# Optimization experiments

Measured on AMD Instinct MI355X. Metric: run time of the kernel, lower is better.

## Reference

```python
import jax, jax.numpy as jnp
import numpy as np

B, C, H, W = 32, 1536, 14, 14   # input is (B*4, C, H, W); joint -> (B, C, 2H, 2W)
CI = C // 2                     # non-local inter_channels
EPS = 1e-5


def conv1x1(x, w, b):
    # x: (b, cin, h, w); w: (cout, cin); b: (cout,)
    return jnp.einsum('bchw,oc->bohw', x, w) + b[None, :, None, None]


def maxpool2(x):
    b, c, h, w = x.shape
    return x.reshape(b, c, h // 2, 2, w // 2, 2).max(axis=(3, 5))


def setup_inputs():
    key = jax.random.key(0)
    ks = jax.random.split(key, 12)
    s = 0.02
    return {
        'x': jax.random.normal(ks[0], (B * 4, C, H, W), jnp.float32),
        'w_theta': jax.random.normal(ks[1], (CI, C), jnp.float32) * s,
        'b_theta': jnp.zeros((CI,), jnp.float32),
        'w_phi': jax.random.normal(ks[2], (CI, C), jnp.float32) * s,
        'b_phi': jnp.zeros((CI,), jnp.float32),
        'w_g': jax.random.normal(ks[3], (CI, C), jnp.float32) * s,
        'b_g': jnp.zeros((CI,), jnp.float32),
        'w_W': jax.random.normal(ks[4], (C, CI), jnp.float32) * s,
        'b_W': jnp.zeros((C,), jnp.float32),
        'bn_gamma': jax.random.normal(ks[5], (C,), jnp.float32) * 0.1 + 1.0,
        'bn_beta': jax.random.normal(ks[6], (C,), jnp.float32) * 0.1,
        'bn_mean': jax.random.normal(ks[7], (C,), jnp.float32) * 0.1,
        'bn_var': jnp.ones((C,), jnp.float32),
    }


def joint(x):
    # (B*4, C, H, W) -> (B, C, 2H, 2W): 4 views tiled in a 2x2 grid
    x4 = x.reshape(B, 4, C, H, W)
    top = jnp.concatenate([x4[:, 0], x4[:, 1]], axis=-1)   # (B, C, H, 2W)
    bot = jnp.concatenate([x4[:, 2], x4[:, 3]], axis=-1)
    return jnp.concatenate([top, bot], axis=-2)             # (B, C, 2H, 2W)


def reference(x, w_theta, b_theta, w_phi, b_phi, w_g, b_g, w_W, b_W,
              bn_gamma, bn_beta, bn_mean, bn_var):
    xj = joint(x)                                           # (B, C, Hj, Wj)
    b, c, hj, wj = xj.shape
    n = hj * wj                                             # 784 query positions

    theta = conv1x1(xj, w_theta, b_theta).reshape(b, CI, n)             # (B, CI, N)
    phi = maxpool2(conv1x1(xj, w_phi, b_phi)).reshape(b, CI, -1)        # (B, CI, N/4)
    g = maxpool2(conv1x1(xj, w_g, b_g)).reshape(b, CI, -1)              # (B, CI, N/4)

    f = jnp.einsum('bcn,bcm->bnm', theta, phi)              # (B, N, N/4)
    attn = jax.nn.softmax(f, axis=-1)
    y = jnp.einsum('bnm,bcm->bcn', attn, g)                 # (B, CI, N)
    y = y.reshape(b, CI, hj, wj)

    w_y = conv1x1(y, w_W, b_W)
    # BatchNorm (inference form)
    inv = jax.lax.rsqrt(bn_var + EPS)
    w_y = (w_y - bn_mean[None, :, None, None]) * (bn_gamma * inv)[None, :, None, None] \
          + bn_beta[None, :, None, None]
    return w_y + xj
```

## Files before the change

kernel.cpp:

```cpp
#include <hip/hip_runtime.h>
#include <hip/hip_bf16.h>

typedef __attribute__((ext_vector_type(8))) _Float16 f16x8;
typedef __attribute__((ext_vector_type(4))) float f32x4;
typedef __attribute__((ext_vector_type(4))) unsigned short us4;
typedef __attribute__((ext_vector_type(8))) unsigned short us8;

#define B_   32
#define C_   1536
#define CI_  768
#define N_   784
#define S_   196
#define MP_  224
#define MK_  196

__device__ __forceinline__ unsigned short f2h(float f) {
    _Float16 h = (_Float16)f;
    return __builtin_bit_cast(unsigned short, h);
}
__device__ __forceinline__ f32x4 mfma_f16(f16x8 a, f16x8 b, f32x4 c) {
    return __builtin_amdgcn_mfma_f32_16x16x32_f16(a, b, c, 0, 0, 0);
}
__device__ __forceinline__ void gl_lds16(const unsigned short* g, unsigned short* l) {
    __builtin_amdgcn_global_load_lds(
        (const __attribute__((address_space(1))) unsigned int*)g,
        (__attribute__((address_space(3))) unsigned int*)l, 16, 0, 0);
}

__global__ __launch_bounds__(256) void k_cvt(const float* __restrict__ src,
                                             unsigned short* __restrict__ dst,
                                             int count4) {
    int idx = blockIdx.x * 256 + threadIdx.x;
    if (idx < count4) {
        f32x4 v = ((const f32x4*)src)[idx];
        us4 o;
        o[0] = f2h(v[0]); o[1] = f2h(v[1]); o[2] = f2h(v[2]); o[3] = f2h(v[3]);
        ((us4*)dst)[idx] = o;
    }
}

__global__ __launch_bounds__(256) void k_build_xjT(const float* __restrict__ x,
                                                   unsigned short* __restrict__ xjT) {
    __shared__ __align__(16) unsigned short lds[196 * 40];
    int c0 = blockIdx.x * 32;
    int b4 = blockIdx.y;
    int b = b4 >> 2, v = b4 & 3;
    int tid = threadIdx.x;
    const float* src = x + ((size_t)b4 * C_ + c0) * S_;
    for (int idx = tid; idx < 32 * 49; idx += 256) {
        int cl = idx / 49;
        int sq = idx - cl * 49;
        f32x4 val = *(const f32x4*)(src + (size_t)cl * S_ + sq * 4);
        int s = sq * 4;
        lds[(s + 0) * 40 + cl] = f2h(val[0]);
        lds[(s + 1) * 40 + cl] = f2h(val[1]);
        lds[(s + 2) * 40 + cl] = f2h(val[2]);
        lds[(s + 3) * 40 + cl] = f2h(val[3]);
    }
    __syncthreads();
    int rowbase = (v >> 1) * 14, colbase = (v & 1) * 14;
    for (int idx = tid; idx < 196 * 4; idx += 256) {
        int s = idx >> 2, ch = idx & 3;
        int hh = s / 14, ww = s - hh * 14;
        int n = (rowbase + hh) * 28 + colbase + ww;
        us8 val = *(const us8*)(&lds[s * 40 + ch * 8]);
        *(us8*)(xjT + ((size_t)b * N_ + n) * C_ + c0 + ch * 8) = val;
    }
}

__global__ __launch_bounds__(256) void k_bnprep(const float* __restrict__ bw,
                                                const float* __restrict__ gamma,
                                                const float* __restrict__ beta,
                                                const float* __restrict__ mean,
                                                const float* __restrict__ var,
                                                float* __restrict__ scale,
                                                float* __restrict__ shift) {
    int i = blockIdx.x * 256 + threadIdx.x;
    if (i < C_) {
        float sc = gamma[i] * rsqrtf(var[i] + 1e-5f);
        scale[i] = sc;
        shift[i] = (bw[i] - mean[i]) * sc + beta[i];
    }
}

__global__ __launch_bounds__(256) void k_conv3(
    const unsigned short* __restrict__ xjT,
    const unsigned short* __restrict__ wf,
    const float* __restrict__ b_theta, const float* __restrict__ b_phi,
    const float* __restrict__ b_g,
    unsigned short* __restrict__ theta_T, unsigned short* __restrict__ phi_p,
    unsigned short* __restrict__ g_p) {
    __shared__ __align__(16) unsigned char smem[28672];
    unsigned short* A_s = (unsigned short*)smem;
    unsigned short* B_s = A_s + 128 * 32;
    float* fLDS = (float*)smem;

    int tn = blockIdx.x;
    int tm = blockIdx.y;
    int b  = blockIdx.z;
    int o0 = tm * 128, n0 = tn * 112;
    int region = o0 / 768;
    int obase = o0 - region * 768;
    const float* bias = (region == 0) ? b_theta : (region == 1) ? b_phi : b_g;

    int tid = threadIdx.x;
    int wv = tid >> 6, lane = tid & 63, lr = lane & 15, quad = lane >> 4;
    int l4r = lane >> 2, l4c = lane & 3;

    f32x4 acc[2][7];
#pragma unroll
    for (int i = 0; i < 2; ++i)
#pragma unroll
        for (int j = 0; j < 7; ++j) acc[i][j] = (f32x4){0.f, 0.f, 0.f, 0.f};

    const unsigned short* Arow = wf + (size_t)o0 * C_;
    const unsigned short* Brow = xjT + ((size_t)b * N_ + n0) * C_;

    for (int kk = 0; kk < 48; ++kk) {
        int k0 = kk * 32;
        for (int c = wv; c < 15; c += 4) {
            if (c < 8) {
                int row = c * 16 + l4r;
                gl_lds16(Arow + (size_t)row * C_ + k0 + l4c * 8, A_s + c * 512);
            } else {
                int cb = c - 8;
                int row = cb * 16 + l4r;
                gl_lds16(Brow + (size_t)row * C_ + k0 + l4c * 8, B_s + cb * 512);
            }
        }
        __syncthreads();
        f16x8 a0 = *(const f16x8*)(&A_s[((2 * wv + 0) * 16 + lr) * 32 + quad * 8]);
        f16x8 a1 = *(const f16x8*)(&A_s[((2 * wv + 1) * 16 + lr) * 32 + quad * 8]);
#pragma unroll
        for (int j = 0; j < 7; ++j) {
            f16x8 bb = *(const f16x8*)(&B_s[(j * 16 + lr) * 32 + quad * 8]);
            acc[0][j] = mfma_f16(a0, bb, acc[0][j]);
            acc[1][j] = mfma_f16(a1, bb, acc[1][j]);
        }
        __syncthreads();
    }

    for (int h = 0; h < 2; ++h) {
        if ((wv >> 1) == h) {
            int wrel = wv & 1;
#pragma unroll
            for (int i = 0; i < 2; ++i)
#pragma unroll
                for (int j = 0; j < 7; ++j)
#pragma unroll
                    for (int r = 0; r < 4; ++r) {
                        int o_rel = (wrel * 2 + i) * 16 + quad * 4 + r;
                        int n_l = j * 16 + lr;
                        fLDS[o_rel * 112 + n_l] = acc[i][j][r];
                    }
        }
        __syncthreads();
        if (region == 0) {
            for (int idx = tid; idx < 112 * 8; idx += 256) {
                int n_l = idx >> 3, ch = idx & 7;
                us8 outv;
#pragma unroll
                for (int k = 0; k < 8; ++k) {
                    int o_rel = ch * 8 + k;
                    float val = fLDS[o_rel * 112 + n_l] + bias[obase + h * 64 + o_rel];
                    outv[k] = f2h(val);
                }
                *(us8*)(theta_T + ((size_t)b * N_ + n0 + n_l) * CI_ + o0 + h * 64 + ch * 8) = outv;
            }
        } else if (region == 1) {
            for (int idx = tid; idx < 28 * 8; idx += 256) {
                int mm = idx >> 3, ch = idx & 7;
                int a = mm / 14, mw = mm - a * 14;
                int m = (tn * 2 + a) * 14 + mw;
                int sb = a * 56 + mw * 2;
                us8 outv;
#pragma unroll
                for (int k = 0; k < 8; ++k) {
                    int o_rel = ch * 8 + k;
                    const float* p = &fLDS[o_rel * 112 + sb];
                    float val = fmaxf(fmaxf(p[0], p[1]), fmaxf(p[28], p[29]));
                    val += bias[obase + h * 64 + o_rel];
                    outv[k] = f2h(val);
                }
                *(us8*)(phi_p + ((size_t)b * MP_ + m) * CI_ + obase + h * 64 + ch * 8) = outv;
            }
        } else {
            for (int idx = tid; idx < 128; idx += 256) {
                int o_rel = idx >> 1, a = idx & 1;
                int ci = obase + h * 64 + o_rel;
                unsigned short* dst = g_p + ((size_t)b * CI_ + ci) * MP_ + (tn * 2 + a) * 14;
                const float* p0 = &fLDS[o_rel * 112 + a * 56];
                float bv = bias[obase + h * 64 + o_rel];
#pragma unroll
                for (int mw = 0; mw < 14; ++mw) {
                    const float* p = p0 + mw * 2;
                    dst[mw] = f2h(fmaxf(fmaxf(p[0], p[1]), fmaxf(p[28], p[29])) + bv);
                }
            }
        }
        __syncthreads();
    }
}

__global__ __launch_bounds__(256) void k_attn(
    const unsigned short* __restrict__ theta_T,
    const unsigned short* __restrict__ phi_p,
    const unsigned short* __restrict__ g_p,
    unsigned short* __restrict__ y) {
    __shared__ __align__(16) float f_s[32 * 228];

    int nb = blockIdx.x, b = blockIdx.y;
    int n0 = nb * 32;
    int tid = threadIdx.x, wv = tid >> 6, lane = tid & 63, lr = lane & 15, quad = lane >> 4;
    int mf0 = wv * 4;
    int nm = (mf0 + 4 <= 14) ? 4 : (14 - mf0);

    int na0 = n0 + lr;       if (na0 > 783) na0 = 783;
    int na1 = n0 + 16 + lr;  if (na1 > 783) na1 = 783;
    const unsigned short* tA0 = theta_T + ((size_t)b * N_ + na0) * CI_ + quad * 8;
    const unsigned short* tA1 = theta_T + ((size_t)b * N_ + na1) * CI_ + quad * 8;

    f32x4 acc[2][4];
#pragma unroll
    for (int i = 0; i < 2; ++i)
#pragma unroll
        for (int j = 0; j < 4; ++j) acc[i][j] = (f32x4){0.f, 0.f, 0.f, 0.f};

    for (int kk = 0; kk < 24; ++kk) {
        int k0 = kk * 32;
        f16x8 a0 = *(const f16x8*)(tA0 + k0);
        f16x8 a1 = *(const f16x8*)(tA1 + k0);
        for (int j = 0; j < nm; ++j) {
            f16x8 bb = *(const f16x8*)(phi_p +
                ((size_t)b * MP_ + (mf0 + j) * 16 + lr) * CI_ + k0 + quad * 8);
            acc[0][j] = mfma_f16(a0, bb, acc[0][j]);
            acc[1][j] = mfma_f16(a1, bb, acc[1][j]);
        }
    }
    for (int i = 0; i < 2; ++i)
        for (int j = 0; j < nm; ++j)
#pragma unroll
            for (int r = 0; r < 4; ++r)
                f_s[(i * 16 + quad * 4 + r) * 228 + (mf0 + j) * 16 + lr] = acc[i][j][r];
    __syncthreads();
    if (tid < 32) {
        float* row = f_s + tid * 228;
        float mx = -1e30f;
        for (int m = 0; m < MK_; ++m) mx = fmaxf(mx, row[m]);
        float sum = 0.f;
        for (int m = 0; m < MK_; ++m) { float e = __expf(row[m] - mx); row[m] = e; sum += e; }
        float inv = 1.0f / sum;
        for (int m = 0; m < MK_; ++m) row[m] *= inv;
        for (int m = MK_; m < MP_; ++m) row[m] = 0.f;
    }
    __syncthreads();
    for (int c3 = 0; c3 < 3; ++c3) {
        int ci0 = c3 * 256;
        f32x4 acc2[2][4];
#pragma unroll
        for (int i = 0; i < 2; ++i)
#pragma unroll
            for (int j = 0; j < 4; ++j) acc2[i][j] = (f32x4){0.f, 0.f, 0.f, 0.f};
        for (int km = 0; km < 7; ++km) {
            int k0 = km * 32;
            f16x8 a[2];
#pragma unroll
            for (int i = 0; i < 2; ++i) {
                const float* fp = &f_s[(i * 16 + lr) * 228 + k0 + quad * 8];
                f16x8 t;
#pragma unroll
                for (int j = 0; j < 8; ++j) t[j] = (_Float16)fp[j];
                a[i] = t;
            }
#pragma unroll
            for (int j = 0; j < 4; ++j) {
                f16x8 bb = *(const f16x8*)(g_p +
                    ((size_t)b * CI_ + ci0 + (wv * 4 + j) * 16 + lr) * MP_ + k0 + quad * 8);
                acc2[0][j] = mfma_f16(a[0], bb, acc2[0][j]);
                acc2[1][j] = mfma_f16(a[1], bb, acc2[1][j]);
            }
        }
#pragma unroll
        for (int i = 0; i < 2; ++i)
#pragma unroll
            for (int j = 0; j < 4; ++j)
#pragma unroll
                for (int r = 0; r < 4; ++r) {
                    int n = n0 + i * 16 + quad * 4 + r;
                    if (n < N_) {
                        int ci = ci0 + (wv * 4 + j) * 16 + lr;
                        y[((size_t)b * N_ + n) * CI_ + ci] = f2h(acc2[i][j][r]);
                    }
                }
    }
}

__global__ __launch_bounds__(256) void k_final(
    const unsigned short* __restrict__ yb,
    const unsigned short* __restrict__ wfW,
    const float* __restrict__ scale, const float* __restrict__ shift,
    const float* __restrict__ x,
    float* __restrict__ out) {
    __shared__ __align__(16) unsigned short smem_us[128 * 32 + 112 * 32];
    unsigned short* A_s = smem_us;
    unsigned short* B_s = smem_us + 128 * 32;
    int tn = blockIdx.x, tm = blockIdx.y, b = blockIdx.z;
    int o0 = tm * 128, n0 = tn * 112;
    int tid = threadIdx.x, wv = tid >> 6, lane = tid & 63, lr = lane & 15, quad = lane >> 4;
    int l4r = lane >> 2, l4c = lane & 3;

    f32x4 acc[2][7];
#pragma unroll
    for (int i = 0; i < 2; ++i)
#pragma unroll
        for (int j = 0; j < 7; ++j) acc[i][j] = (f32x4){0.f, 0.f, 0.f, 0.f};

    const unsigned short* Arow = wfW + (size_t)o0 * CI_;
    const unsigned short* Brow = yb + ((size_t)b * N_ + n0) * CI_;

    for (int kk = 0; kk < 24; ++kk) {
        int k0 = kk * 32;
        for (int c = wv; c < 15; c += 4) {
            if (c < 8) {
                int row = c * 16 + l4r;
                gl_lds16(Arow + (size_t)row * CI_ + k0 + l4c * 8, A_s + c * 512);
            } else {
                int cb = c - 8;
                int row = cb * 16 + l4r;
                gl_lds16(Brow + (size_t)row * CI_ + k0 + l4c * 8, B_s + cb * 512);
            }
        }
        __syncthreads();
        f16x8 a0 = *(const f16x8*)(&A_s[((2 * wv + 0) * 16 + lr) * 32 + quad * 8]);
        f16x8 a1 = *(const f16x8*)(&A_s[((2 * wv + 1) * 16 + lr) * 32 + quad * 8]);
#pragma unroll
        for (int j = 0; j < 7; ++j) {
            f16x8 bb = *(const f16x8*)(&B_s[(j * 16 + lr) * 32 + quad * 8]);
            acc[0][j] = mfma_f16(a0, bb, acc[0][j]);
            acc[1][j] = mfma_f16(a1, bb, acc[1][j]);
        }
        __syncthreads();
    }
#pragma unroll
    for (int i = 0; i < 2; ++i)
#pragma unroll
        for (int r = 0; r < 4; ++r) {
            int o = o0 + (2 * wv + i) * 16 + quad * 4 + r;
            float sc = scale[o], sh = shift[o];
#pragma unroll
            for (int j = 0; j < 7; ++j) {
                int n = n0 + j * 16 + lr;
                int hh = n / 28, ww = n - hh * 28;
                int vv = ((hh >= 14) ? 2 : 0) + ((ww >= 14) ? 1 : 0);
                int s = (hh - ((hh >= 14) ? 14 : 0)) * 14 + (ww - ((ww >= 14) ? 14 : 0));
                float xval = x[((size_t)(b * 4 + vv) * C_ + o) * S_ + s];
                out[((size_t)b * C_ + o) * N_ + n] = acc[i][j][r] * sc + sh + xval;
            }
        }
}

extern "C" void kernel_launch(void* const* d_in, const int* in_sizes, int n_in,
                              void* d_out, int out_size, void* d_ws, size_t ws_size,
                              hipStream_t stream) {
    (void)in_sizes; (void)n_in; (void)out_size; (void)ws_size;
    const float* x       = (const float*)d_in[0];
    const float* w_theta = (const float*)d_in[1];
    const float* b_theta = (const float*)d_in[2];
    const float* w_phi   = (const float*)d_in[3];
    const float* b_phi   = (const float*)d_in[4];
    const float* w_g     = (const float*)d_in[5];
    const float* b_g     = (const float*)d_in[6];
    const float* w_W     = (const float*)d_in[7];
    const float* b_W     = (const float*)d_in[8];
    const float* gamma   = (const float*)d_in[9];
    const float* beta    = (const float*)d_in[10];
    const float* mean    = (const float*)d_in[11];
    const float* var     = (const float*)d_in[12];

    char* ob = (char*)d_out;
    unsigned short* xjT     = (unsigned short*)(ob);
    unsigned short* theta_T = (unsigned short*)(ob + 77070336);
    unsigned short* phi_p   = (unsigned short*)(ob + 115605504);
    unsigned short* g_p     = (unsigned short*)(ob + 126615552);
    unsigned short* wf3     = (unsigned short*)(ob + 137625600);

    char* ws = (char*)d_ws;
    unsigned short* yb    = (unsigned short*)(ws);
    unsigned short* wfW   = (unsigned short*)(ws + 38535168);
    float*          scale = (float*)(ws + 40894464);
    float*          shift = (float*)(ws + 40900608);

    hipMemsetAsync(phi_p, 0, 11010048, stream);
    hipMemsetAsync(g_p, 0, 11010048, stream);

    k_bnprep<<<6, 256, 0, stream>>>(b_W, gamma, beta, mean, var, scale, shift);
    k_cvt<<<1152, 256, 0, stream>>>(w_theta, wf3,                294912);
    k_cvt<<<1152, 256, 0, stream>>>(w_phi,   wf3 + 768 * 1536,   294912);
    k_cvt<<<1152, 256, 0, stream>>>(w_g,     wf3 + 2 * 768 * 1536, 294912);
    k_cvt<<<1152, 256, 0, stream>>>(w_W,     wfW,                294912);
    k_build_xjT<<<dim3(48, 128), 256, 0, stream>>>(x, xjT);
    k_conv3<<<dim3(7, 18, 32), 256, 0, stream>>>(xjT, wf3, b_theta, b_phi, b_g,
                                                 theta_T, phi_p, g_p);
    k_attn<<<dim3(25, 32), 256, 0, stream>>>(theta_T, phi_p, g_p, yb);
    k_final<<<dim3(7, 12, 32), 256, 0, stream>>>(yb, wfW, scale, shift, x,
                                                 (float*)d_out);
}
```

Before: 882.7 us.

## Double-buffer LDS staging with XOR swizzle in GEMMs and parallelize softmax rows

Both 1x1-conv GEMM kernels now use two LDS buffers, so the global-to-LDS load of the next K slice is issued before computing on the current one. This replaces the load/sync/compute/sync serialization. An XOR swizzle on the 16-byte column chunk is applied to reads and writes to reduce LDS bank conflicts. The attention softmax now spreads each row over 8 threads with shuffle reductions instead of 32 serial threads, which costs more LDS and relies on the async loads completing before the barrier.

```diff
diff --git a/kernel.cpp b/kernel.cpp
--- a/kernel.cpp
+++ b/kernel.cpp
@@ -25,6 +25,23 @@
     __builtin_amdgcn_global_load_lds(
         (const __attribute__((address_space(1))) unsigned int*)g,
         (__attribute__((address_space(3))) unsigned int*)l, 16, 0, 0);
+}
+
+__device__ __forceinline__ void stage15(const unsigned short* Arow,
+                                        const unsigned short* Brow,
+                                        unsigned short* A_s, unsigned short* B_s,
+                                        int k0, int stride,
+                                        int wv, int l4r, int l4c_sw) {
+    for (int c = wv; c < 15; c += 4) {
+        if (c < 8) {
+            gl_lds16(Arow + (size_t)(c * 16 + l4r) * stride + k0 + l4c_sw * 8,
+                     A_s + c * 512);
+        } else {
+            int cb = c - 8;
+            gl_lds16(Brow + (size_t)(cb * 16 + l4r) * stride + k0 + l4c_sw * 8,
+                     B_s + cb * 512);
+        }
+    }
 }
 
 __global__ __launch_bounds__(256) void k_cvt(const float* __restrict__ src,
@@ -83,6 +100,18 @@
     }
 }
 
+#define COMPUTE_STEP(As, Bs)                                                     \
+    {                                                                            \
+        f16x8 a0 = *(const f16x8*)(&(As)[((2 * wv + 0) * 16 + lr) * 32 + rcol]); \
+        f16x8 a1 = *(const f16x8*)(&(As)[((2 * wv + 1) * 16 + lr) * 32 + rcol]); \
+        _Pragma("unroll")                                                        \
+        for (int j = 0; j < 7; ++j) {                                            \
+            f16x8 bb = *(const f16x8*)(&(Bs)[(j * 16 + lr) * 32 + rcol]);        \
+            acc[0][j] = mfma_f16(a0, bb, acc[0][j]);                             \
+            acc[1][j] = mfma_f16(a1, bb, acc[1][j]);                             \
+        }                                                                        \
+    }
+
 __global__ __launch_bounds__(256) void k_conv3(
     const unsigned short* __restrict__ xjT,
     const unsigned short* __restrict__ wf,
@@ -90,9 +119,11 @@
     const float* __restrict__ b_g,
     unsigned short* __restrict__ theta_T, unsigned short* __restrict__ phi_p,
     unsigned short* __restrict__ g_p) {
-    __shared__ __align__(16) unsigned char smem[28672];
-    unsigned short* A_s = (unsigned short*)smem;
-    unsigned short* B_s = A_s + 128 * 32;
+    __shared__ __align__(16) unsigned char smem[30720];
+    unsigned short* A0 = (unsigned short*)smem;
+    unsigned short* B0 = A0 + 4096;
+    unsigned short* A1 = A0 + 7680;
+    unsigned short* B1 = A0 + 11776;
     float* fLDS = (float*)smem;
 
     int tn = blockIdx.x;
@@ -106,6 +137,8 @@
     int tid = threadIdx.x;
     int wv = tid >> 6, lane = tid & 63, lr = lane & 15, quad = lane >> 4;
     int l4r = lane >> 2, l4c = lane & 3;
+    int l4c_sw = l4c ^ ((l4r >> 1) & 3);
+    int rcol = (quad ^ ((lr >> 1) & 3)) * 8;
 
     f32x4 acc[2][7];
 #pragma unroll
@@ -116,27 +149,15 @@
     const unsigned short* Arow = wf + (size_t)o0 * C_;
     const unsigned short* Brow = xjT + ((size_t)b * N_ + n0) * C_;
 
-    for (int kk = 0; kk < 48; ++kk) {
-        int k0 = kk * 32;
-        for (int c = wv; c < 15; c += 4) {
-            if (c < 8) {
-                int row = c * 16 + l4r;
-                gl_lds16(Arow + (size_t)row * C_ + k0 + l4c * 8, A_s + c * 512);
-            } else {
-                int cb = c - 8;
-                int row = cb * 16 + l4r;
-                gl_lds16(Brow + (size_t)row * C_ + k0 + l4c * 8, B_s + cb * 512);
-            }
-        }
-        __syncthreads();
-        f16x8 a0 = *(const f16x8*)(&A_s[((2 * wv + 0) * 16 + lr) * 32 + quad * 8]);
-        f16x8 a1 = *(const f16x8*)(&A_s[((2 * wv + 1) * 16 + lr) * 32 + quad * 8]);
-#pragma unroll
-        for (int j = 0; j < 7; ++j) {
-            f16x8 bb = *(const f16x8*)(&B_s[(j * 16 + lr) * 32 + quad * 8]);
-            acc[0][j] = mfma_f16(a0, bb, acc[0][j]);
-            acc[1][j] = mfma_f16(a1, bb, acc[1][j]);
-        }
+    stage15(Arow, Brow, A0, B0, 0, C_, wv, l4r, l4c_sw);
+    __syncthreads();
+    for (int kk = 0; kk < 48; kk += 2) {
+        stage15(Arow, Brow, A1, B1, (kk + 1) * 32, C_, wv, l4r, l4c_sw);
+        COMPUTE_STEP(A0, B0);
+        __syncthreads();
+        if (kk + 2 < 48)
+            stage15(Arow, Brow, A0, B0, (kk + 2) * 32, C_, wv, l4r, l4c_sw);
+        COMPUTE_STEP(A1, B1);
         __syncthreads();
     }
 
@@ -243,15 +264,30 @@
             for (int r = 0; r < 4; ++r)
                 f_s[(i * 16 + quad * 4 + r) * 228 + (mf0 + j) * 16 + lr] = acc[i][j][r];
     __syncthreads();
-    if (tid < 32) {
-        float* row = f_s + tid * 228;
+    {
+        int row = tid >> 3, sub = tid & 7;
+        float* rowp = f_s + row * 228;
+        int m0 = sub * 28;
         float mx = -1e30f;
-        for (int m = 0; m < MK_; ++m) mx = fmaxf(mx, row[m]);
+#pragma unroll
+        for (int m = 0; m < 28; ++m)
+            if (m0 + m < MK_) mx = fmaxf(mx, rowp[m0 + m]);
+        mx = fmaxf(mx, __shfl_xor(mx, 1));
+        mx = fmaxf(mx, __shfl_xor(mx, 2));
+        mx = fmaxf(mx, __shfl_xor(mx, 4));
         float sum = 0.f;
-        for (int m = 0; m < MK_; ++m) { float e = __expf(row[m] - mx); row[m] = e; sum += e; }
+#pragma unroll
+        for (int m = 0; m < 28; ++m) {
+            float e = (m0 + m < MK_) ? __expf(rowp[m0 + m] - mx) : 0.f;
+            rowp[m0 + m] = e;
+            sum += e;
+        }
+        sum += __shfl_xor(sum, 1);
+        sum += __shfl_xor(sum, 2);
+        sum += __shfl_xor(sum, 4);
         float inv = 1.0f / sum;
-        for (int m = 0; m < MK_; ++m) row[m] *= inv;
-        for (int m = MK_; m < MP_; ++m) row[m] = 0.f;
+#pragma unroll
+        for (int m = 0; m < 28; ++m) rowp[m0 + m] *= inv;
     }
     __syncthreads();
     for (int c3 = 0; c3 < 3; ++c3) {
@@ -301,13 +337,17 @@
     const float* __restrict__ scale, const float* __restrict__ shift,
     const float* __restrict__ x,
     float* __restrict__ out) {
-    __shared__ __align__(16) unsigned short smem_us[128 * 32 + 112 * 32];
-    unsigned short* A_s = smem_us;
-    unsigned short* B_s = smem_us + 128 * 32;
+    __shared__ __align__(16) unsigned short smem_us[2 * (128 * 32 + 112 * 32)];
+    unsigned short* A0 = smem_us;
+    unsigned short* B0 = smem_us + 4096;
+    unsigned short* A1 = smem_us + 7680;
+    unsigned short* B1 = smem_us + 11776;
     int tn = blockIdx.x, tm = blockIdx.y, b = blockIdx.z;
     int o0 = tm * 128, n0 = tn * 112;
     int tid = threadIdx.x, wv = tid >> 6, lane = tid & 63, lr = lane & 15, quad = lane >> 4;
     int l4r = lane >> 2, l4c = lane & 3;
+    int l4c_sw = l4c ^ ((l4r >> 1) & 3);
+    int rcol = (quad ^ ((lr >> 1) & 3)) * 8;
 
     f32x4 acc[2][7];
 #pragma unroll
@@ -318,27 +358,15 @@
     const unsigned short* Arow = wfW + (size_t)o0 * CI_;
     const unsigned short* Brow = yb + ((size_t)b * N_ + n0) * CI_;
 
-    for (int kk = 0; kk < 24; ++kk) {
-        int k0 = kk * 32;
-        for (int c = wv; c < 15; c += 4) {
-            if (c < 8) {
-                int row = c * 16 + l4r;
-                gl_lds16(Arow + (size_t)row * CI_ + k0 + l4c * 8, A_s + c * 512);
-            } else {
-                int cb = c - 8;
-                int row = cb * 16 + l4r;
-                gl_lds16(Brow + (size_t)row * CI_ + k0 + l4c * 8, B_s + cb * 512);
-            }
-        }
-        __syncthreads();
-        f16x8 a0 = *(const f16x8*)(&A_s[((2 * wv + 0) * 16 + lr) * 32 + quad * 8]);
-        f16x8 a1 = *(const f16x8*)(&A_s[((2 * wv + 1) * 16 + lr) * 32 + quad * 8]);
-#pragma unroll
-        for (int j = 0; j < 7; ++j) {
-            f16x8 bb = *(const f16x8*)(&B_s[(j * 16 + lr) * 32 + quad * 8]);
-            acc[0][j] = mfma_f16(a0, bb, acc[0][j]);
-            acc[1][j] = mfma_f16(a1, bb, acc[1][j]);
-        }
+    stage15(Arow, Brow, A0, B0, 0, CI_, wv, l4r, l4c_sw);
+    __syncthreads();
+    for (int kk = 0; kk < 24; kk += 2) {
+        stage15(Arow, Brow, A1, B1, (kk + 1) * 32, CI_, wv, l4r, l4c_sw);
+        COMPUTE_STEP(A0, B0);
+        __syncthreads();
+        if (kk + 2 < 24)
+            stage15(Arow, Brow, A0, B0, (kk + 2) * 32, CI_, wv, l4r, l4c_sw);
+        COMPUTE_STEP(A1, B1);
         __syncthreads();
     }
 #pragma unroll
```

Result: no change. 867.5 us (-1.7%).
